# Performance work log

Hardware: AMD Instinct MI355X
Metric: run time of the kernel (lower is better)

The kernel has to match this reference:

```python
import jax, jax.numpy as jnp
import numpy as np

NODE_F = 8      # node_features
HID = 128       # hidden_dim
HEADS = 8       # nn.MultiheadAttention num_heads
OUT = 256       # output_dim
MAX_ATOMS = 4096  # max_pocket_atoms
NEIGHBOR_RADIUS = 3.0   # _compute_surface_scores neighbor_radius


def setup_inputs() -> dict:
    key = jax.random.key(0)
    ks = jax.random.split(key, 16)
    N, M = 16384, 32
    x = jax.random.normal(ks[0], (N, NODE_F), dtype=jnp.float32)
    pos = jax.random.normal(ks[1], (N, 3), dtype=jnp.float32) * 10.0
    ligand_pos = jax.random.normal(ks[2], (M, 3), dtype=jnp.float32) * 3.0

    def lin(k, fan_in, fan_out):
        return jax.random.normal(k, (fan_in, fan_out), dtype=jnp.float32) / np.sqrt(fan_in)

    return {
        'x': x, 'pos': pos, 'ligand_pos': ligand_pos,
        'W_node': lin(ks[3], NODE_F, HID), 'b_node': jnp.zeros((HID,), jnp.float32),
        'Wq': lin(ks[4], HID, HID), 'bq': jnp.zeros((HID,), jnp.float32),
        'Wk': lin(ks[5], HID, HID), 'bk': jnp.zeros((HID,), jnp.float32),
        'Wv': lin(ks[6], HID, HID), 'bv': jnp.zeros((HID,), jnp.float32),
        'Wo': lin(ks[7], HID, HID), 'bo': jnp.zeros((HID,), jnp.float32),
        'W1': lin(ks[8], HID, OUT), 'b1': jnp.zeros((OUT,), jnp.float32),
        'W2': lin(ks[9], OUT, OUT), 'b2': jnp.zeros((OUT,), jnp.float32),
    }


def _select_binding_site(pos, ligand_pos, k):
    # select_by_binding_site_proximity: distance-to-ligand-center + surface scores, topk
    lig_center = jnp.mean(ligand_pos, axis=0)                       # [3]
    d_lig = jnp.linalg.norm(pos - lig_center, axis=1)               # [N]
    # _compute_surface_scores: cdist(pos,pos) < 3.0, count neighbors (minus self)
    sq = jnp.sum(pos * pos, axis=1)                                 # [N]
    d2 = sq[:, None] + sq[None, :] - 2.0 * (pos @ pos.T)            # [N,N] squared distances
    neighbor_counts = jnp.sum(d2 < NEIGHBOR_RADIUS ** 2, axis=1) - 1
    surface = 1.0 / (neighbor_counts.astype(jnp.float32) + 1.0)
    scores = 1.0 / (1.0 + d_lig / 5.0) + 0.5 * surface
    _, idx = jax.lax.top_k(scores, k)                               # largest=True
    return idx


def reference(x, pos, ligand_pos, W_node, b_node, Wq, bq, Wk, bk, Wv, bv, Wo, bo, W1, b1, W2, b2):
    # N > max_pocket_atoms -> smart selection (adaptive with ligand_pos => binding_site)
    idx = _select_binding_site(pos, ligand_pos, MAX_ATOMS)
    xs = x[idx]                                                     # [K, NODE_F]

    # node embedding (E3 net call fails in the original -> h = node_embedding(x))
    h = xs @ W_node + b_node                                        # [K, HID]

    # MultiheadAttention over the single (batch=None) sequence, eval mode (no dropout)
    K = MAX_ATOMS
    dh = HID // HEADS
    q = (h @ Wq + bq).reshape(K, HEADS, dh).transpose(1, 0, 2)      # [H,K,dh]
    k_ = (h @ Wk + bk).reshape(K, HEADS, dh).transpose(1, 0, 2)
    v = (h @ Wv + bv).reshape(K, HEADS, dh).transpose(1, 0, 2)
    attn = jax.nn.softmax(jnp.einsum('hqd,hkd->hqk', q, k_) / np.sqrt(dh), axis=-1)
    av = jnp.einsum('hqk,hkd->hqd', attn, v).transpose(1, 0, 2).reshape(K, HID)
    h_att = av @ Wo + bo                                            # [K, HID]

    # global mean pool + output projection (Linear-ReLU-Linear)
    pooled = jnp.mean(h_att, axis=0)                                # [HID]
    out = jax.nn.relu(pooled @ W1 + b1) @ W2 + b2                   # [OUT]
    return out
```

## Files before the change

### kernel.cpp

```cpp
#include <hip/hip_runtime.h>
#include <cstdint>
#include <cstddef>

#define NPTS 16384
#define KSEL 4096
#define HIDDEN 128
#define NHEADS 8
#define DHEAD 16
#define OUTD 256
#define NSLICE 4
#define FCAP 131072
#define LCAP 2048
#define TAU 0.2f

typedef __attribute__((ext_vector_type(8))) short bf16x8;
typedef __attribute__((ext_vector_type(4))) float f32x4;

#if defined(__has_builtin)
#if __has_builtin(__builtin_amdgcn_exp2f)
#define E2(x) __builtin_amdgcn_exp2f(x)
#endif
#endif
#ifndef E2
#define E2(x) exp2f(x)
#endif

constexpr size_t OFF_PA    = 1024;
constexpr size_t OFF_PB    = OFF_PA  + (size_t)NPTS*32;
constexpr size_t OFF_SQ    = OFF_PB  + (size_t)NPTS*32;
constexpr size_t OFF_DL    = OFF_SQ  + (size_t)NPTS*4;
constexpr size_t OFF_CNT   = OFF_DL  + (size_t)NPTS*4;
constexpr size_t OFF_NFLAG = OFF_CNT + (size_t)NPTS*4;
constexpr size_t OFF_FLG   = OFF_NFLAG + 1024;
constexpr size_t OFF_SEL   = OFF_FLG + (size_t)FCAP*4;
constexpr size_t SZ_PK     = (size_t)NHEADS*KSEL*32*2;
constexpr size_t OFF_QPK   = OFF_SEL + (size_t)KSEL*4;
constexpr size_t OFF_KPK   = OFF_QPK + SZ_PK;
constexpr size_t OFF_V     = OFF_KPK + SZ_PK;
constexpr size_t OFF_LP    = OFF_V  + (size_t)KSEL*HIDDEN*4;
constexpr size_t OFF_RL    = OFF_LP + (size_t)NHEADS*KSEL*NSLICE*4;
constexpr size_t OFF_WP    = OFF_RL + (size_t)NHEADS*KSEL*4;
constexpr size_t OFF_PAV   = OFF_WP + (size_t)NHEADS*KSEL*NSLICE*4;

__device__ __forceinline__ unsigned short f2bf(float f) {
    union { float f; unsigned u; } v; v.f = f;
    unsigned r = v.u + 0x7fffu + ((v.u >> 16) & 1u);
    return (unsigned short)(r >> 16);
}
__device__ __forceinline__ float bf2f(unsigned short h) {
    union { unsigned u; float f; } v; v.u = ((unsigned)h) << 16;
    return v.f;
}

__global__ void __launch_bounds__(256) k_prep(const float* __restrict__ pos, const float* __restrict__ lig, int M,
                       unsigned short* __restrict__ pa, unsigned short* __restrict__ pb,
                       float* __restrict__ sq, float* __restrict__ dl) {
    __shared__ float ls[128];
    __shared__ float ctr[3];
    int tid = threadIdx.x;
    for (int i = tid; i < 3 * M; i += 256) ls[i] = lig[i];
    __syncthreads();
    if (tid < 3) {
        float s = 0.f;
        for (int i = 0; i < M; i++) s += ls[i * 3 + tid];
        ctr[tid] = s / (float)M;
    }
    __syncthreads();
    int i = blockIdx.x * 256 + tid;
    float x = pos[i*3+0], y = pos[i*3+1], z = pos[i*3+2];
    float s = (x*x + y*y) + z*z;
    sq[i] = s;
    float dx = x - ctr[0], dy = y - ctr[1], dz = z - ctr[2];
    dl[i] = sqrtf((dx*dx + dy*dy) + dz*dz);
    unsigned short xh = f2bf(x); float xr = bf2f(xh); float xl = x - xr;
    unsigned short yh = f2bf(y); float yr = bf2f(yh); float yl = y - yr;
    unsigned short zh = f2bf(z); float zr = bf2f(zh); float zl = z - zr;
    unsigned short xlb = f2bf(xl), ylb = f2bf(yl), zlb = f2bf(zl);
    unsigned short xhA = f2bf(-2.f*xr), xlA = f2bf(-2.f*xl);
    unsigned short yhA = f2bf(-2.f*yr), ylA = f2bf(-2.f*yl);
    unsigned short zhA = f2bf(-2.f*zr), zlA = f2bf(-2.f*zl);
    unsigned short sih = f2bf(s);
    unsigned short sil = f2bf(s - bf2f(sih));
    unsigned short one = f2bf(1.0f);
    union { unsigned short s[16]; float4 f[2]; } A, B;
    A.s[0]=xhA; A.s[1]=xhA; A.s[2]=xlA;
    A.s[3]=yhA; A.s[4]=yhA; A.s[5]=ylA;
    A.s[6]=zhA; A.s[7]=zhA; A.s[8]=zlA;
    A.s[9]=xlA; A.s[10]=ylA; A.s[11]=zlA;
    A.s[12]=sih; A.s[13]=sil; A.s[14]=one; A.s[15]=one;
    B.s[0]=xh;  B.s[1]=xlb;  B.s[2]=xh;
    B.s[3]=yh;  B.s[4]=ylb;  B.s[5]=yh;
    B.s[6]=zh;  B.s[7]=zlb;  B.s[8]=zh;
    B.s[9]=xlb; B.s[10]=ylb; B.s[11]=zlb;
    B.s[12]=one; B.s[13]=one; B.s[14]=sih; B.s[15]=sil;
    float4* pad = (float4*)(pa + (size_t)i * 16);
    pad[0] = A.f[0]; pad[1] = A.f[1];
    float4* pbd = (float4*)(pb + (size_t)i * 16);
    pbd[0] = B.f[0]; pbd[1] = B.f[1];
}

__global__ void __launch_bounds__(256) k_neighbor(
        const unsigned short* __restrict__ pa, const unsigned short* __restrict__ pb,
        int* __restrict__ cnt, unsigned int* __restrict__ flg, unsigned int* __restrict__ nflag) {
    __shared__ unsigned short bs[256 * 24];
    __shared__ unsigned int fbuf[LCAP];
    __shared__ unsigned int fcnt, fbase;
    int tid = threadIdx.x;
    if (tid == 0) fcnt = 0;
    int lane = tid & 63, w = tid >> 6;
    int n = lane & 15, g = lane >> 4;
    int i0 = blockIdx.x * 64 + w * 16;
    bf16x8 afrag = {0,0,0,0,0,0,0,0};
    if (g < 2) afrag = *(const bf16x8*)(pa + (size_t)(i0 + n) * 16 + g * 8);
    int irow = i0 + g * 4;
    int boff = (g < 2) ? g * 8 : 0;
    int jb0 = blockIdx.y * 4096;
    int c0 = 0, c1 = 0, c2 = 0, c3 = 0;
    for (int ch = 0; ch < 16; ch++) {
        __syncthreads();
        {
            const float4* src = (const float4*)(pb + (size_t)(jb0 + ch*256 + tid) * 16);
            float4 v0 = src[0], v1 = src[1];
            float4* dst = (float4*)&bs[tid * 24];
            dst[0] = v0; dst[1] = v1;
        }
        __syncthreads();
        int jb = jb0 + ch * 256;
        #pragma unroll 4
        for (int t = 0; t < 16; t++) {
            int jj = t * 16 + n;
            bf16x8 bfrag = *(const bf16x8*)&bs[jj * 24 + boff];
            f32x4 c = {0.f, 0.f, 0.f, 0.f};
            c = __builtin_amdgcn_mfma_f32_16x16x32_bf16(afrag, bfrag, c, 0, 0, 0);
            float d0 = c[0] - 9.0f, d1 = c[1] - 9.0f, d2_ = c[2] - 9.0f, d3 = c[3] - 9.0f;
            bool a0 = d0 < -TAU, a1 = d1 < -TAU, a2 = d2_ < -TAU, a3 = d3 < -TAU;
            bool f0 = (d0 < TAU) && !a0, f1 = (d1 < TAU) && !a1;
            bool f2 = (d2_ < TAU) && !a2, f3 = (d3 < TAU) && !a3;
            c0 += a0; c1 += a1; c2 += a2; c3 += a3;
            if (f0 | f1 | f2 | f3) {
                int j = jb + jj;
                if (f0) { unsigned xx = atomicAdd(&fcnt, 1u); if (xx < LCAP) fbuf[xx] = ((unsigned)(irow+0) << 14) | (unsigned)j; }
                if (f1) { unsigned xx = atomicAdd(&fcnt, 1u); if (xx < LCAP) fbuf[xx] = ((unsigned)(irow+1) << 14) | (unsigned)j; }
                if (f2) { unsigned xx = atomicAdd(&fcnt, 1u); if (xx < LCAP) fbuf[xx] = ((unsigned)(irow+2) << 14) | (unsigned)j; }
                if (f3) { unsigned xx = atomicAdd(&fcnt, 1u); if (xx < LCAP) fbuf[xx] = ((unsigned)(irow+3) << 14) | (unsigned)j; }
            }
        }
    }
    #pragma unroll
    for (int m = 1; m < 16; m <<= 1) {
        c0 += __shfl_xor(c0, m); c1 += __shfl_xor(c1, m);
        c2 += __shfl_xor(c2, m); c3 += __shfl_xor(c3, m);
    }
    if (n == 0) {
        atomicAdd(&cnt[irow+0], c0);
        atomicAdd(&cnt[irow+1], c1);
        atomicAdd(&cnt[irow+2], c2);
        atomicAdd(&cnt[irow+3], c3);
    }
    __syncthreads();
    if (tid == 0) {
        unsigned cf = fcnt; if (cf > LCAP) cf = LCAP;
        fcnt = cf;
        fbase = atomicAdd(nflag, cf);
    }
    __syncthreads();
    unsigned cf = fcnt, fb = fbase;
    for (unsigned xx = tid; xx < cf; xx += 256) {
        unsigned di = fb + xx;
        if (di < FCAP) flg[di] = fbuf[xx];
    }
}

__global__ void __launch_bounds__(256) k_fixup(const float* __restrict__ pos, const float* __restrict__ sq,
        const unsigned int* __restrict__ flg, const unsigned int* __restrict__ nflag,
        int* __restrict__ cnt) {
    int nf = (int)*nflag; if (nf > FCAP) nf = FCAP;
    for (int idx = blockIdx.x * 256 + threadIdx.x; idx < nf; idx += gridDim.x * 256) {
        unsigned pr = flg[idx];
        int i = (int)(pr >> 14), j = (int)(pr & 16383u);
        float xi = pos[i*3+0], yi = pos[i*3+1], zi = pos[i*3+2];
        float xj = pos[j*3+0], yj = pos[j*3+1], zj = pos[j*3+2];
        float dot = fmaf(xi, xj, fmaf(yi, yj, zi * zj));
        float d2 = (sq[i] + sq[j]) - 2.0f * dot;
        if (d2 < 9.0f) atomicAdd(&cnt[i], 1);
    }
}

__global__ void __launch_bounds__(1024) k_select(const float* __restrict__ dl, const int* __restrict__ cnt,
                                                 int* __restrict__ sel) {
    __shared__ unsigned int sk[NPTS];
    __shared__ int hist[256];
    __shared__ int scan2[256];
    __shared__ unsigned int s_prefix;
    __shared__ int s_rem, s_eqtot, s_nout, s_digit, s_cgt;
    int tid = threadIdx.x;
    for (int i = tid; i < NPTS; i += 1024) {
        float score = 1.0f / (1.0f + dl[i] / 5.0f) + 0.5f * (1.0f / (float)cnt[i]);
        unsigned int u = __float_as_uint(score);
        sk[i] = u ^ ((u & 0x80000000u) ? 0xFFFFFFFFu : 0x80000000u);
    }
    if (tid == 0) { s_prefix = 0; s_rem = KSEL; s_nout = 0; s_eqtot = 0; }
    __syncthreads();
    for (int p = 0; p < 4; p++) {
        int sh = 24 - 8 * p;
        if (tid < 256) hist[tid] = 0;
        __syncthreads();
        unsigned int pref = s_prefix;
        int shp = (p == 0) ? 0 : (32 - 8 * p);
        for (int i = tid; i < NPTS; i += 1024) {
            unsigned int key = sk[i];
            bool m = (p == 0) || ((key >> shp) == pref);
            if (m) atomicAdd(&hist[(key >> sh) & 255], 1);
        }
        __syncthreads();
        if (tid < 256) scan2[tid] = hist[tid];
        __syncthreads();
        for (int off = 1; off < 256; off <<= 1) {
            int v = 0;
            if (tid < 256) { v = scan2[tid]; if (tid + off < 256) v += scan2[tid + off]; }
            __syncthreads();
            if (tid < 256) scan2[tid] = v;
            __syncthreads();
        }
        int rem = s_rem;
        if (tid < 256) {
            int hi = scan2[tid];
            int lo = hi - hist[tid];
            if (hi >= rem && lo < rem) { s_digit = tid; s_cgt = lo; }
        }
        __syncthreads();
        if (tid == 0) {
            s_prefix = (s_prefix << 8) | (unsigned int)s_digit;
            s_rem = rem - s_cgt;
            if (p == 3) s_eqtot = hist[s_digit];
        }
        __syncthreads();
    }
    unsigned int T = s_prefix;
    int need_eq = s_rem;
    for (int i = tid; i < NPTS; i += 1024)
        if (sk[i] > T) sel[atomicAdd(&s_nout, 1)] = i;
    __syncthreads();
    if (s_eqtot == need_eq) {
        for (int i = tid; i < NPTS; i += 1024)
            if (sk[i] == T) sel[atomicAdd(&s_nout, 1)] = i;
    } else {
        for (int i = tid; i < NPTS; i += 1024) {
            if (sk[i] == T) {
                int rank = 0;
                for (int j = 0; j < i; j++) rank += (sk[j] == T);
                if (rank < need_eq) sel[atomicAdd(&s_nout, 1)] = i;
            }
        }
    }
}

__device__ __forceinline__ void proj8(const float hs[8][HIDDEN], const float* __restrict__ W,
                                      float b, int d, float* acc) {
    #pragma unroll
    for (int r = 0; r < 8; r++) acc[r] = b;
    for (int c = 0; c < HIDDEN; c += 4) {
        float w0 = W[(c+0)*HIDDEN+d], w1 = W[(c+1)*HIDDEN+d], w2 = W[(c+2)*HIDDEN+d], w3 = W[(c+3)*HIDDEN+d];
        #pragma unroll
        for (int r = 0; r < 8; r++) {
            float4 h4 = *(const float4*)&hs[r][c];
            float a = acc[r];
            a = fmaf(h4.x, w0, a); a = fmaf(h4.y, w1, a); a = fmaf(h4.z, w2, a); a = fmaf(h4.w, w3, a);
            acc[r] = a;
        }
    }
}

__global__ void __launch_bounds__(128) k_qkv(const float* __restrict__ x, const int* __restrict__ sel,
        const float* __restrict__ Wn, const float* __restrict__ bn,
        const float* __restrict__ Wq, const float* __restrict__ bq,
        const float* __restrict__ Wk, const float* __restrict__ bk,
        const float* __restrict__ Wv, const float* __restrict__ bv,
        unsigned short* __restrict__ qpk, unsigned short* __restrict__ kpk,
        float* __restrict__ vg) {
    __shared__ float xs[8][8];
    __shared__ __align__(16) float hs[8][HIDDEN];
    int d = threadIdx.x;
    int r0 = blockIdx.x * 8;
    if (d < 64) { int rr = d >> 3, cc = d & 7; xs[rr][cc] = x[(size_t)sel[r0 + rr] * 8 + cc]; }
    __syncthreads();
    {
        float wn[8];
        #pragma unroll
        for (int c = 0; c < 8; c++) wn[c] = Wn[c * HIDDEN + d];
        float b = bn[d];
        #pragma unroll
        for (int r = 0; r < 8; r++) {
            float a = b;
            #pragma unroll
            for (int c = 0; c < 8; c++) a = fmaf(xs[r][c], wn[c], a);
            hs[r][d] = a;
        }
    }
    __syncthreads();
    int hh = d >> 4, dd = d & 15;
    float acc[8];
    proj8(hs, Wq, bq[d], d, acc);
    #pragma unroll
    for (int r = 0; r < 8; r++) {
        float val = acc[r] * 0.36067376022224085f;
        unsigned short hi = f2bf(val);
        unsigned short lo = f2bf(val - bf2f(hi));
        size_t idx = ((size_t)(hh * KSEL) + r0 + r) * 32 + dd;
        qpk[idx] = hi; qpk[idx + 16] = lo;
    }
    proj8(hs, Wk, bk[d], d, acc);
    #pragma unroll
    for (int r = 0; r < 8; r++) {
        float val = acc[r];
        unsigned short hi = f2bf(val);
        unsigned short lo = f2bf(val - bf2f(hi));
        size_t idx = ((size_t)(hh * KSEL) + r0 + r) * 32 + dd;
        kpk[idx] = hi; kpk[idx + 16] = lo;
    }
    proj8(hs, Wv, bv[d], d, acc);
    #pragma unroll
    for (int r = 0; r < 8; r++) vg[(size_t)(r0+r)*HIDDEN + d] = acc[r];
}

__global__ void __launch_bounds__(256) k_attn_l(
        const unsigned short* __restrict__ qpk, const unsigned short* __restrict__ kpk,
        float* __restrict__ lp) {
    __shared__ unsigned short smem[256 * 40];
    int tid = threadIdx.x;
    int ks = blockIdx.x, yg = blockIdx.y, h = blockIdx.z;
    size_t hb = (size_t)h * KSEL;
    int lane = tid & 63, w = tid >> 6;
    int n = lane & 15, g = lane >> 4;
    int q0w = yg * 64 + w * 16;
    bf16x8 afrag = *(const bf16x8*)(qpk + (hb + q0w + n) * 32 + g * 8);
    float l0 = 0.f, l1 = 0.f, l2 = 0.f, l3 = 0.f;
    int b1off = (g & 1) * 8;
    int b2off = 16 + g * 8;
    for (int kc = 0; kc < 4; kc++) {
        __syncthreads();
        {
            int krow = ks * 1024 + kc * 256 + tid;
            const float4* src = (const float4*)(kpk + (hb + krow) * 32);
            float4 a0 = src[0], a1 = src[1], a2 = src[2], a3 = src[3];
            float4* dst = (float4*)&smem[tid * 40];
            dst[0] = a0; dst[1] = a1; dst[2] = a2; dst[3] = a3;
        }
        __syncthreads();
        #pragma unroll 4
        for (int t = 0; t < 16; t++) {
            const unsigned short* rowp = &smem[(t * 16 + n) * 40];
            bf16x8 b1 = *(const bf16x8*)(rowp + b1off);
            bf16x8 b2 = {0,0,0,0,0,0,0,0};
            if (g < 2) b2 = *(const bf16x8*)(rowp + b2off);
            f32x4 c = {0.f, 0.f, 0.f, 0.f};
            c = __builtin_amdgcn_mfma_f32_16x16x32_bf16(afrag, b1, c, 0, 0, 0);
            c = __builtin_amdgcn_mfma_f32_16x16x32_bf16(afrag, b2, c, 0, 0, 0);
            l0 += E2(c[0]); l1 += E2(c[1]); l2 += E2(c[2]); l3 += E2(c[3]);
        }
    }
    #pragma unroll
    for (int m = 1; m < 16; m <<= 1) {
        l0 += __shfl_xor(l0, m); l1 += __shfl_xor(l1, m);
        l2 += __shfl_xor(l2, m); l3 += __shfl_xor(l3, m);
    }
    if (n == 0) {
        size_t base = (hb + q0w + g * 4) * NSLICE + ks;
        lp[base]            = l0; lp[base + NSLICE]     = l1;
        lp[base + 2*NSLICE] = l2; lp[base + 3*NSLICE]   = l3;
    }
}

__global__ void k_rl(const float* __restrict__ lp, float* __restrict__ rl) {
    int i = blockIdx.x * 256 + threadIdx.x;
    float4 p = ((const float4*)lp)[i];
    rl[i] = 1.0f / ((p.x + p.y) + (p.z + p.w));
}

__global__ void __launch_bounds__(256) k_attn_w(
        const unsigned short* __restrict__ qpk, const unsigned short* __restrict__ kpk,
        const float* __restrict__ rl, float* __restrict__ wp) {
    __shared__ unsigned short smem[256 * 40];
    __shared__ float rls[256];
    int tid = threadIdx.x;
    int qs = blockIdx.x, yg = blockIdx.y, h = blockIdx.z;
    size_t hb = (size_t)h * KSEL;
    int lane = tid & 63, w = tid >> 6;
    int n = lane & 15, g = lane >> 4;
    int j0w = yg * 64 + w * 16;
    bf16x8 afrag = *(const bf16x8*)(kpk + (hb + j0w + n) * 32 + g * 8);
    float w0 = 0.f, w1 = 0.f, w2 = 0.f, w3 = 0.f;
    int b1off = (g & 1) * 8;
    int b2off = 16 + g * 8;
    for (int qc = 0; qc < 4; qc++) {
        __syncthreads();
        {
            int qrow = qs * 1024 + qc * 256 + tid;
            const float4* src = (const float4*)(qpk + (hb + qrow) * 32);
            float4 a0 = src[0], a1 = src[1], a2 = src[2], a3 = src[3];
            float4* dst = (float4*)&smem[tid * 40];
            dst[0] = a0; dst[1] = a1; dst[2] = a2; dst[3] = a3;
            rls[tid] = rl[hb + qrow];
        }
        __syncthreads();
        #pragma unroll 4
        for (int t = 0; t < 16; t++) {
            const unsigned short* rowp = &smem[(t * 16 + n) * 40];
            bf16x8 b1 = *(const bf16x8*)(rowp + b1off);
            bf16x8 b2 = {0,0,0,0,0,0,0,0};
            if (g < 2) b2 = *(const bf16x8*)(rowp + b2off);
            f32x4 c = {0.f, 0.f, 0.f, 0.f};
            c = __builtin_amdgcn_mfma_f32_16x16x32_bf16(afrag, b1, c, 0, 0, 0);
            c = __builtin_amdgcn_mfma_f32_16x16x32_bf16(afrag, b2, c, 0, 0, 0);
            float rv = rls[t * 16 + n];
            w0 = fmaf(E2(c[0]), rv, w0); w1 = fmaf(E2(c[1]), rv, w1);
            w2 = fmaf(E2(c[2]), rv, w2); w3 = fmaf(E2(c[3]), rv, w3);
        }
    }
    #pragma unroll
    for (int m = 1; m < 16; m <<= 1) {
        w0 += __shfl_xor(w0, m); w1 += __shfl_xor(w1, m);
        w2 += __shfl_xor(w2, m); w3 += __shfl_xor(w3, m);
    }
    if (n == 0) {
        size_t base = (hb + j0w + g * 4) * NSLICE + qs;
        wp[base]            = w0; wp[base + NSLICE]     = w1;
        wp[base + 2*NSLICE] = w2; wp[base + 3*NSLICE]   = w3;
    }
}

__global__ void __launch_bounds__(256) k_colsum(const float* __restrict__ wp, const float* __restrict__ vg,
                                                float* __restrict__ pav) {
    __shared__ float wl[NHEADS][128];
    __shared__ float red[128];
    int tid = threadIdx.x;
    int jb = blockIdx.x * 128;
    for (int i = tid; i < NHEADS * 128; i += 256) {
        int h = i >> 7, jl = i & 127;
        float4 p = ((const float4*)wp)[(size_t)h * KSEL + jb + jl];
        wl[h][jl] = (p.x + p.y) + (p.z + p.w);
    }
    __syncthreads();
    int d = tid & 127, g = tid >> 7;
    int h = d >> 4;
    float acc = 0.f;
    for (int jl = g * 64; jl < g * 64 + 64; jl++)
        acc = fmaf(wl[h][jl], vg[(size_t)(jb + jl) * HIDDEN + d], acc);
    if (g == 1) red[d] = acc;
    __syncthreads();
    if (g == 0) atomicAdd(&pav[d], (acc + red[d]) * (1.0f / (float)KSEL));
}

__global__ void __launch_bounds__(256) k_final(const float* __restrict__ pav,
        const float* __restrict__ Wo, const float* __restrict__ bo,
        const float* __restrict__ W1, const float* __restrict__ b1,
        const float* __restrict__ W2, const float* __restrict__ b2,
        float* __restrict__ out) {
    __shared__ float sp[HIDDEN];
    __shared__ float st[OUTD];
    int t = threadIdx.x;
    if (t < HIDDEN) {
        float a = bo[t];
        for (int c = 0; c < HIDDEN; c++) a = fmaf(pav[c], Wo[c * HIDDEN + t], a);
        sp[t] = a;
    }
    __syncthreads();
    {
        float a = b1[t];
        for (int c = 0; c < HIDDEN; c++) a = fmaf(sp[c], W1[c * OUTD + t], a);
        st[t] = fmaxf(a, 0.f);
    }
    __syncthreads();
    {
        float o = b2[t];
        for (int c = 0; c < OUTD; c++) o = fmaf(st[c], W2[c * OUTD + t], o);
        out[t] = o;
    }
}

extern "C" void kernel_launch(void* const* d_in, const int* in_sizes, int n_in,
                              void* d_out, int out_size, void* d_ws, size_t ws_size,
                              hipStream_t stream) {
    (void)n_in; (void)out_size; (void)ws_size;
    const float* x   = (const float*)d_in[0];
    const float* pos = (const float*)d_in[1];
    const float* lig = (const float*)d_in[2];
    const float* Wn  = (const float*)d_in[3];
    const float* bn  = (const float*)d_in[4];
    const float* Wq  = (const float*)d_in[5];
    const float* bq  = (const float*)d_in[6];
    const float* Wk  = (const float*)d_in[7];
    const float* bk  = (const float*)d_in[8];
    const float* Wv  = (const float*)d_in[9];
    const float* bv  = (const float*)d_in[10];
    const float* Wo  = (const float*)d_in[11];
    const float* bo  = (const float*)d_in[12];
    const float* W1  = (const float*)d_in[13];
    const float* b1  = (const float*)d_in[14];
    const float* W2  = (const float*)d_in[15];
    const float* b2  = (const float*)d_in[16];
    int M = in_sizes[2] / 3;

    char* ws = (char*)d_ws;
    unsigned short* pa  = (unsigned short*)(ws + OFF_PA);
    unsigned short* pb  = (unsigned short*)(ws + OFF_PB);
    float*          sq  = (float*)(ws + OFF_SQ);
    float*          dl  = (float*)(ws + OFF_DL);
    int*            cnt = (int*)  (ws + OFF_CNT);
    unsigned int*   nfl = (unsigned int*)(ws + OFF_NFLAG);
    unsigned int*   flg = (unsigned int*)(ws + OFF_FLG);
    int*            sel = (int*)  (ws + OFF_SEL);
    unsigned short* qpk = (unsigned short*)(ws + OFF_QPK);
    unsigned short* kpk = (unsigned short*)(ws + OFF_KPK);
    float*          vg  = (float*)(ws + OFF_V);
    float*          lp  = (float*)(ws + OFF_LP);
    float*          rl  = (float*)(ws + OFF_RL);
    float*          wp  = (float*)(ws + OFF_WP);
    float*          pav = (float*)(ws + OFF_PAV);

    hipMemsetAsync(ws + OFF_CNT, 0, (size_t)NPTS * 4 + 1024, stream);
    hipMemsetAsync(ws + OFF_PAV, 0, (size_t)HIDDEN * 4, stream);

    hipLaunchKernelGGL(k_prep,     dim3(64),       dim3(256),  0, stream, pos, lig, M, pa, pb, sq, dl);
    hipLaunchKernelGGL(k_neighbor, dim3(256, 4),   dim3(256),  0, stream, pa, pb, cnt, flg, nfl);
    hipLaunchKernelGGL(k_fixup,    dim3(32),       dim3(256),  0, stream, pos, sq, flg, nfl, cnt);
    hipLaunchKernelGGL(k_select,   dim3(1),        dim3(1024), 0, stream, dl, cnt, sel);
    hipLaunchKernelGGL(k_qkv,      dim3(KSEL/8),   dim3(128),  0, stream, x, sel, Wn, bn, Wq, bq, Wk, bk, Wv, bv, qpk, kpk, vg);
    hipLaunchKernelGGL(k_attn_l,   dim3(4, 64, 8), dim3(256),  0, stream, qpk, kpk, lp);
    hipLaunchKernelGGL(k_rl,       dim3(NHEADS*KSEL/256), dim3(256), 0, stream, lp, rl);
    hipLaunchKernelGGL(k_attn_w,   dim3(4, 64, 8), dim3(256),  0, stream, qpk, kpk, rl, wp);
    hipLaunchKernelGGL(k_colsum,   dim3(32),       dim3(256),  0, stream, wp, vg, pav);
    hipLaunchKernelGGL(k_final,    dim3(1),        dim3(256),  0, stream, pav, Wo, bo, W1, b1, W2, b2, (float*)d_out);
}
```

Baseline: 301.2 us.

## Exploit distance symmetry in neighbor counting and shrink QKV rows per block

The neighbor-count kernel now computes only the upper-triangular tiles of the pairwise distance matrix. Each off-diagonal tile hit is also credited to the column point through a shared-memory column counter, and borderline pairs are flagged so the fixup kernel increments both endpoints. This roughly halves the MFMA distance work, at the cost of extra shuffles, LDS atomics and unbalanced blocks, since many grid blocks exit early. Separately, the QKV projection kernel handles 4 rows per block instead of 8, launching twice as many blocks for more parallelism.

New measurement: 294.4 us. -2.3%, faster.

```diff
diff --git a/kernel.cpp b/kernel.cpp
--- a/kernel.cpp
+++ b/kernel.cpp
@@ -102,47 +102,60 @@
 __global__ void __launch_bounds__(256) k_neighbor(
         const unsigned short* __restrict__ pa, const unsigned short* __restrict__ pb,
         int* __restrict__ cnt, unsigned int* __restrict__ flg, unsigned int* __restrict__ nflag) {
+    int s = blockIdx.x, ch = blockIdx.y;
+    int jb0 = ch * 2048;
+    if (jb0 + 2048 <= s * 64) return;
     __shared__ unsigned short bs[256 * 24];
+    __shared__ int colcnt[2048];
     __shared__ unsigned int fbuf[LCAP];
     __shared__ unsigned int fcnt, fbase;
     int tid = threadIdx.x;
+    for (int i = tid; i < 2048; i += 256) colcnt[i] = 0;
     if (tid == 0) fcnt = 0;
     int lane = tid & 63, w = tid >> 6;
     int n = lane & 15, g = lane >> 4;
-    int i0 = blockIdx.x * 64 + w * 16;
+    int i0 = s * 64 + w * 16;
     bf16x8 afrag = {0,0,0,0,0,0,0,0};
     if (g < 2) afrag = *(const bf16x8*)(pa + (size_t)(i0 + n) * 16 + g * 8);
     int irow = i0 + g * 4;
     int boff = (g < 2) ? g * 8 : 0;
-    int jb0 = blockIdx.y * 4096;
     int c0 = 0, c1 = 0, c2 = 0, c3 = 0;
-    for (int ch = 0; ch < 16; ch++) {
+    for (int sub = 0; sub < 8; sub++) {
+        int jb = jb0 + sub * 256;
+        if (jb + 256 <= s * 64) continue;
         __syncthreads();
         {
-            const float4* src = (const float4*)(pb + (size_t)(jb0 + ch*256 + tid) * 16);
+            const float4* src = (const float4*)(pb + (size_t)(jb + tid) * 16);
             float4 v0 = src[0], v1 = src[1];
             float4* dst = (float4*)&bs[tid * 24];
             dst[0] = v0; dst[1] = v1;
         }
         __syncthreads();
-        int jb = jb0 + ch * 256;
-        #pragma unroll 4
         for (int t = 0; t < 16; t++) {
-            int jj = t * 16 + n;
-            bf16x8 bfrag = *(const bf16x8*)&bs[jj * 24 + boff];
+            int jt = jb + t * 16;
+            if (jt < i0) continue;
+            bool sym = (jt > i0);
+            bf16x8 bfrag = *(const bf16x8*)&bs[(t * 16 + n) * 24 + boff];
             f32x4 c = {0.f, 0.f, 0.f, 0.f};
             c = __builtin_amdgcn_mfma_f32_16x16x32_bf16(afrag, bfrag, c, 0, 0, 0);
-            float d0 = c[0] - 9.0f, d1 = c[1] - 9.0f, d2_ = c[2] - 9.0f, d3 = c[3] - 9.0f;
-            bool a0 = d0 < -TAU, a1 = d1 < -TAU, a2 = d2_ < -TAU, a3 = d3 < -TAU;
-            bool f0 = (d0 < TAU) && !a0, f1 = (d1 < TAU) && !a1;
-            bool f2 = (d2_ < TAU) && !a2, f3 = (d3 < TAU) && !a3;
+            bool a0 = c[0] < (9.0f - TAU), a1 = c[1] < (9.0f - TAU);
+            bool a2 = c[2] < (9.0f - TAU), a3 = c[3] < (9.0f - TAU);
+            bool f0 = (c[0] < 9.0f + TAU) && !a0, f1 = (c[1] < 9.0f + TAU) && !a1;
+            bool f2 = (c[2] < 9.0f + TAU) && !a2, f3 = (c[3] < 9.0f + TAU) && !a3;
             c0 += a0; c1 += a1; c2 += a2; c3 += a3;
+            if (sym) {
+                int sl = (int)a0 + (int)a1 + (int)a2 + (int)a3;
+                sl += __shfl_xor(sl, 16);
+                sl += __shfl_xor(sl, 32);
+                if (g == 0 && sl != 0) atomicAdd(&colcnt[jt - jb0 + n], sl);
+            }
             if (f0 | f1 | f2 | f3) {
-                int j = jb + jj;
-                if (f0) { unsigned xx = atomicAdd(&fcnt, 1u); if (xx < LCAP) fbuf[xx] = ((unsigned)(irow+0) << 14) | (unsigned)j; }
-                if (f1) { unsigned xx = atomicAdd(&fcnt, 1u); if (xx < LCAP) fbuf[xx] = ((unsigned)(irow+1) << 14) | (unsigned)j; }
-                if (f2) { unsigned xx = atomicAdd(&fcnt, 1u); if (xx < LCAP) fbuf[xx] = ((unsigned)(irow+2) << 14) | (unsigned)j; }
-                if (f3) { unsigned xx = atomicAdd(&fcnt, 1u); if (xx < LCAP) fbuf[xx] = ((unsigned)(irow+3) << 14) | (unsigned)j; }
+                unsigned sb = sym ? (1u << 28) : 0u;
+                int j = jt + n;
+                if (f0) { unsigned xx = atomicAdd(&fcnt, 1u); if (xx < LCAP) fbuf[xx] = sb | ((unsigned)(irow+0) << 14) | (unsigned)j; }
+                if (f1) { unsigned xx = atomicAdd(&fcnt, 1u); if (xx < LCAP) fbuf[xx] = sb | ((unsigned)(irow+1) << 14) | (unsigned)j; }
+                if (f2) { unsigned xx = atomicAdd(&fcnt, 1u); if (xx < LCAP) fbuf[xx] = sb | ((unsigned)(irow+2) << 14) | (unsigned)j; }
+                if (f3) { unsigned xx = atomicAdd(&fcnt, 1u); if (xx < LCAP) fbuf[xx] = sb | ((unsigned)(irow+3) << 14) | (unsigned)j; }
             }
         }
     }
@@ -152,12 +165,16 @@
         c2 += __shfl_xor(c2, m); c3 += __shfl_xor(c3, m);
     }
     if (n == 0) {
-        atomicAdd(&cnt[irow+0], c0);
-        atomicAdd(&cnt[irow+1], c1);
-        atomicAdd(&cnt[irow+2], c2);
-        atomicAdd(&cnt[irow+3], c3);
-    }
-    __syncthreads();
+        if (c0) atomicAdd(&cnt[irow+0], c0);
+        if (c1) atomicAdd(&cnt[irow+1], c1);
+        if (c2) atomicAdd(&cnt[irow+2], c2);
+        if (c3) atomicAdd(&cnt[irow+3], c3);
+    }
+    __syncthreads();
+    for (int i = tid; i < 2048; i += 256) {
+        int v = colcnt[i];
+        if (v) atomicAdd(&cnt[jb0 + i], v);
+    }
     if (tid == 0) {
         unsigned cf = fcnt; if (cf > LCAP) cf = LCAP;
         fcnt = cf;
@@ -177,12 +194,15 @@
     int nf = (int)*nflag; if (nf > FCAP) nf = FCAP;
     for (int idx = blockIdx.x * 256 + threadIdx.x; idx < nf; idx += gridDim.x * 256) {
         unsigned pr = flg[idx];
-        int i = (int)(pr >> 14), j = (int)(pr & 16383u);
+        int i = (int)((pr >> 14) & 16383u), j = (int)(pr & 16383u);
         float xi = pos[i*3+0], yi = pos[i*3+1], zi = pos[i*3+2];
         float xj = pos[j*3+0], yj = pos[j*3+1], zj = pos[j*3+2];
         float dot = fmaf(xi, xj, fmaf(yi, yj, zi * zj));
         float d2 = (sq[i] + sq[j]) - 2.0f * dot;
-        if (d2 < 9.0f) atomicAdd(&cnt[i], 1);
+        if (d2 < 9.0f) {
+            atomicAdd(&cnt[i], 1);
+            if (pr & (1u << 28)) atomicAdd(&cnt[j], 1);
+        }
     }
 }
 
@@ -255,14 +275,14 @@
     }
 }
 
-__device__ __forceinline__ void proj8(const float hs[8][HIDDEN], const float* __restrict__ W,
+__device__ __forceinline__ void proj4(const float hs[4][HIDDEN], const float* __restrict__ W,
                                       float b, int d, float* acc) {
     #pragma unroll
-    for (int r = 0; r < 8; r++) acc[r] = b;
+    for (int r = 0; r < 4; r++) acc[r] = b;
     for (int c = 0; c < HIDDEN; c += 4) {
         float w0 = W[(c+0)*HIDDEN+d], w1 = W[(c+1)*HIDDEN+d], w2 = W[(c+2)*HIDDEN+d], w3 = W[(c+3)*HIDDEN+d];
         #pragma unroll
-        for (int r = 0; r < 8; r++) {
+        for (int r = 0; r < 4; r++) {
             float4 h4 = *(const float4*)&hs[r][c];
             float a = acc[r];
             a = fmaf(h4.x, w0, a); a = fmaf(h4.y, w1, a); a = fmaf(h4.z, w2, a); a = fmaf(h4.w, w3, a);
@@ -278,11 +298,11 @@
         const float* __restrict__ Wv, const float* __restrict__ bv,
         unsigned short* __restrict__ qpk, unsigned short* __restrict__ kpk,
         float* __restrict__ vg) {
-    __shared__ float xs[8][8];
-    __shared__ __align__(16) float hs[8][HIDDEN];
+    __shared__ float xs[4][8];
+    __shared__ __align__(16) float hs[4][HIDDEN];
     int d = threadIdx.x;
-    int r0 = blockIdx.x * 8;
-    if (d < 64) { int rr = d >> 3, cc = d & 7; xs[rr][cc] = x[(size_t)sel[r0 + rr] * 8 + cc]; }
+    int r0 = blockIdx.x * 4;
+    if (d < 32) { int rr = d >> 3, cc = d & 7; xs[rr][cc] = x[(size_t)sel[r0 + rr] * 8 + cc]; }
     __syncthreads();
     {
         float wn[8];
@@ -290,7 +310,7 @@
         for (int c = 0; c < 8; c++) wn[c] = Wn[c * HIDDEN + d];
         float b = bn[d];
         #pragma unroll
-        for (int r = 0; r < 8; r++) {
+        for (int r = 0; r < 4; r++) {
             float a = b;
             #pragma unroll
             for (int c = 0; c < 8; c++) a = fmaf(xs[r][c], wn[c], a);
@@ -299,28 +319,28 @@
     }
     __syncthreads();
     int hh = d >> 4, dd = d & 15;
-    float acc[8];
-    proj8(hs, Wq, bq[d], d, acc);
-    #pragma unroll
-    for (int r = 0; r < 8; r++) {
+    float acc[4];
+    proj4(hs, Wq, bq[d], d, acc);
+    #pragma unroll
+    for (int r = 0; r < 4; r++) {
         float val = acc[r] * 0.36067376022224085f;
         unsigned short hi = f2bf(val);
         unsigned short lo = f2bf(val - bf2f(hi));
         size_t idx = ((size_t)(hh * KSEL) + r0 + r) * 32 + dd;
         qpk[idx] = hi; qpk[idx + 16] = lo;
     }
-    proj8(hs, Wk, bk[d], d, acc);
-    #pragma unroll
-    for (int r = 0; r < 8; r++) {
+    proj4(hs, Wk, bk[d], d, acc);
+    #pragma unroll
+    for (int r = 0; r < 4; r++) {
         float val = acc[r];
         unsigned short hi = f2bf(val);
         unsigned short lo = f2bf(val - bf2f(hi));
         size_t idx = ((size_t)(hh * KSEL) + r0 + r) * 32 + dd;
         kpk[idx] = hi; kpk[idx + 16] = lo;
     }
-    proj8(hs, Wv, bv[d], d, acc);
-    #pragma unroll
-    for (int r = 0; r < 8; r++) vg[(size_t)(r0+r)*HIDDEN + d] = acc[r];
+    proj4(hs, Wv, bv[d], d, acc);
+    #pragma unroll
+    for (int r = 0; r < 4; r++) vg[(size_t)(r0+r)*HIDDEN + d] = acc[r];
 }
 
 __global__ void __launch_bounds__(256) k_attn_l(
@@ -522,10 +542,10 @@
     hipMemsetAsync(ws + OFF_PAV, 0, (size_t)HIDDEN * 4, stream);
 
     hipLaunchKernelGGL(k_prep,     dim3(64),       dim3(256),  0, stream, pos, lig, M, pa, pb, sq, dl);
-    hipLaunchKernelGGL(k_neighbor, dim3(256, 4),   dim3(256),  0, stream, pa, pb, cnt, flg, nfl);
+    hipLaunchKernelGGL(k_neighbor, dim3(256, 8),   dim3(256),  0, stream, pa, pb, cnt, flg, nfl);
     hipLaunchKernelGGL(k_fixup,    dim3(32),       dim3(256),  0, stream, pos, sq, flg, nfl, cnt);
     hipLaunchKernelGGL(k_select,   dim3(1),        dim3(1024), 0, stream, dl, cnt, sel);
-    hipLaunchKernelGGL(k_qkv,      dim3(KSEL/8),   dim3(128),  0, stream, x, sel, Wn, bn, Wq, bq, Wk, bk, Wv, bv, qpk, kpk, vg);
+    hipLaunchKernelGGL(k_qkv,      dim3(KSEL/4),   dim3(128),  0, stream, x, sel, Wn, bn, Wq, bq, Wk, bk, Wv, bv, qpk, kpk, vg);
     hipLaunchKernelGGL(k_attn_l,   dim3(4, 64, 8), dim3(256),  0, stream, qpk, kpk, lp);
     hipLaunchKernelGGL(k_rl,       dim3(NHEADS*KSEL/256), dim3(256), 0, stream, lp, rl);
     hipLaunchKernelGGL(k_attn_w,   dim3(4, 64, 8), dim3(256),  0, stream, qpk, kpk, rl, wp);
```
